# Performance work log

Measured on AMD Instinct MI355X. Metric: run time of the kernel, lower is better.

## Reference

```python
import jax, jax.numpy as jnp
import numpy as np

B, S, D, H = 2, 2048, 1024, 16
HD = D // H  # head_dim = 64


def setup_inputs() -> dict:
    key = jax.random.key(0)
    ks = jax.random.split(key, 6)
    sc = 1.0 / np.sqrt(D)
    x = jax.random.normal(ks[0], (B, S, D), dtype=jnp.float32)
    # causal boolean mask, broadcast over heads: [B, 1, S, S]
    causal = jnp.tril(jnp.ones((S, S), dtype=bool))
    attn_mask = jnp.broadcast_to(causal[None, None], (B, 1, S, S))
    return {
        "x": x,
        "attn_mask": attn_mask,
        "Wq": jax.random.normal(ks[1], (D, D), dtype=jnp.float32) * sc,
        "bq": jnp.zeros((D,), dtype=jnp.float32),
        "Wk": jax.random.normal(ks[2], (D, D), dtype=jnp.float32) * sc,
        "bk": jnp.zeros((D,), dtype=jnp.float32),
        "Wv": jax.random.normal(ks[3], (D, D), dtype=jnp.float32) * sc,
        "bv": jnp.zeros((D,), dtype=jnp.float32),
        "Wo": jax.random.normal(ks[4], (D, D), dtype=jnp.float32) * sc,
        "bo": jnp.zeros((D,), dtype=jnp.float32),
    }


def _split_heads(t):
    # [B, S, D] -> [B, H, S, HD]
    return t.reshape(B, S, H, HD).transpose(0, 2, 1, 3)


def reference(x, attn_mask, Wq, bq, Wk, bk, Wv, bv, Wo, bo):
    q = _split_heads(x @ Wq + bq)
    k = _split_heads(x @ Wk + bk)
    v = _split_heads(x @ Wv + bv)
    scale = 1.0 / jnp.sqrt(jnp.asarray(HD, dtype=x.dtype))
    # [B, H, S, S] scores
    scores = jnp.einsum("bhqd,bhkd->bhqk", q, k) * scale
    scores = jnp.where(attn_mask, scores, jnp.asarray(-jnp.inf, dtype=x.dtype))
    probs = jax.nn.softmax(scores, axis=-1)
    out = jnp.einsum("bhqk,bhkd->bhqd", probs, v)  # [B, H, S, HD]
    out = out.transpose(0, 2, 1, 3).reshape(B, S, D)
    return out @ Wo + bo
```

## Files before the change

### kernel.cpp

```cpp
#include <hip/hip_runtime.h>
#include <math.h>

#define BB 2
#define SS 2048
#define DDIM 1024
#define HH 16
#define HD 64
#define MM (BB * SS)

typedef short s16x8 __attribute__((ext_vector_type(8)));
typedef short s16x4 __attribute__((ext_vector_type(4)));
typedef float f32x4 __attribute__((ext_vector_type(4)));
typedef unsigned int u32x4 __attribute__((ext_vector_type(4)));

__device__ __forceinline__ unsigned short f2bf(float f) {
    unsigned int u = __builtin_bit_cast(unsigned int, f);
    u += 0x7fffu + ((u >> 16) & 1u);
    return (unsigned short)(u >> 16);
}
__device__ __forceinline__ float bf2f(unsigned short h) {
    return __builtin_bit_cast(float, (unsigned int)h << 16);
}

__global__ __launch_bounds__(256) void wsplit(
    const float* __restrict__ W0, const float* __restrict__ W1,
    const float* __restrict__ W2, const float* __restrict__ W3,
    short* __restrict__ WtH, short* __restrict__ WtL)
{
    __shared__ float T[64][65];
    const int z  = blockIdx.z;
    const float* W = (z == 0) ? W0 : (z == 1) ? W1 : (z == 2) ? W2 : W3;
    const int n0 = blockIdx.x * 64;
    const int k0 = blockIdx.y * 64;
    const int t  = threadIdx.x;

#pragma unroll
    for (int i = 0; i < 4; ++i) {
        const int kr = (t >> 4) + i * 16;
        const int c4 = (t & 15) * 4;
        const float4 v = *(const float4*)&W[(size_t)(k0 + kr) * DDIM + n0 + c4];
        T[kr][c4 + 0] = v.x; T[kr][c4 + 1] = v.y;
        T[kr][c4 + 2] = v.z; T[kr][c4 + 3] = v.w;
    }
    __syncthreads();

    const int n  = t >> 2;
    const int kb = (t & 3) * 16;
    s16x8 h0, h1, l0, l1;
#pragma unroll
    for (int j = 0; j < 8; ++j) {
        const float f0 = T[kb + j][n];
        const unsigned short hh0 = f2bf(f0);
        h0[j] = (short)hh0; l0[j] = (short)f2bf(f0 - bf2f(hh0));
        const float f1 = T[kb + 8 + j][n];
        const unsigned short hh1 = f2bf(f1);
        h1[j] = (short)hh1; l1[j] = (short)f2bf(f1 - bf2f(hh1));
    }
    const size_t ob = ((size_t)z * DDIM + n0 + n) * DDIM + k0 + kb;
    *(s16x8*)&WtH[ob]     = h0;
    *(s16x8*)&WtH[ob + 8] = h1;
    *(s16x8*)&WtL[ob]     = l0;
    *(s16x8*)&WtL[ob + 8] = l1;
}

template <int MODE>
__global__ __launch_bounds__(256) void proj_v2(
    const float* __restrict__ A, const short* __restrict__ BTh,
    const short* __restrict__ BTl, const float* __restrict__ bias,
    void* __restrict__ Cout)
{
    __shared__ short Bh[64 * 64];
    __shared__ short Bl[64 * 64];

    const int tid  = threadIdx.x;
    const int lane = tid & 63;
    const int wave = tid >> 6;
    const int g    = lane >> 4;
    const int qq   = lane & 15;
    const int wm   = (wave >> 1) * 32;
    const int wn   = (wave & 1) * 32;
    const int n0   = blockIdx.x * 64;
    const int m0   = blockIdx.y * 64;

    const int sr = tid >> 2;
    const int sc = (tid & 3) * 2;
    const int d0 = sr * 64 + ((sc ^ (sr & 7)) * 8);
    const int d1 = sr * 64 + (((sc + 1) ^ (sr & 7)) * 8);

    f32x4 acc[2][2];
#pragma unroll
    for (int i = 0; i < 2; ++i)
#pragma unroll
        for (int j = 0; j < 2; ++j) acc[i][j] = (f32x4){0.f, 0.f, 0.f, 0.f};

    for (int kt = 0; kt < 16; ++kt) {
        const int k0 = kt * 64;
        __syncthreads();
        {
            const size_t gb = (size_t)(n0 + sr) * DDIM + k0 + sc * 8;
            const s16x8 h0 = *(const s16x8*)&BTh[gb];
            const s16x8 h1 = *(const s16x8*)&BTh[gb + 8];
            const s16x8 l0 = *(const s16x8*)&BTl[gb];
            const s16x8 l1 = *(const s16x8*)&BTl[gb + 8];
            *(s16x8*)&Bh[d0] = h0;
            *(s16x8*)&Bh[d1] = h1;
            *(s16x8*)&Bl[d0] = l0;
            *(s16x8*)&Bl[d1] = l1;
        }
        __syncthreads();

#pragma unroll
        for (int ks = 0; ks < 2; ++ks) {
            s16x8 bhf[2], blf[2];
#pragma unroll
            for (int nf = 0; nf < 2; ++nf) {
                const int r  = wn + 16 * nf + qq;
                const int ch = (((ks * 4 + g) ^ (qq & 7)) * 8);
                bhf[nf] = *(const s16x8*)&Bh[r * 64 + ch];
                blf[nf] = *(const s16x8*)&Bl[r * 64 + ch];
            }
#pragma unroll
            for (int mf = 0; mf < 2; ++mf) {
                const float* ap = &A[(size_t)(m0 + wm + 16 * mf + qq) * DDIM + k0 + ks * 32 + g * 8];
                const float4 a0 = *(const float4*)ap;
                const float4 a1 = *(const float4*)(ap + 4);
                const float av[8] = {a0.x, a0.y, a0.z, a0.w, a1.x, a1.y, a1.z, a1.w};
                s16x8 ah, al;
#pragma unroll
                for (int i = 0; i < 8; ++i) {
                    const unsigned short hh = f2bf(av[i]);
                    ah[i] = (short)hh;
                    al[i] = (short)f2bf(av[i] - bf2f(hh));
                }
#pragma unroll
                for (int nf = 0; nf < 2; ++nf) {
                    acc[mf][nf] = __builtin_amdgcn_mfma_f32_16x16x32_bf16(ah, bhf[nf], acc[mf][nf], 0, 0, 0);
                    acc[mf][nf] = __builtin_amdgcn_mfma_f32_16x16x32_bf16(ah, blf[nf], acc[mf][nf], 0, 0, 0);
                    acc[mf][nf] = __builtin_amdgcn_mfma_f32_16x16x32_bf16(al, bhf[nf], acc[mf][nf], 0, 0, 0);
                }
            }
        }
    }

    float bv2[2];
#pragma unroll
    for (int nf = 0; nf < 2; ++nf) bv2[nf] = bias[n0 + wn + 16 * nf + qq];

#pragma unroll
    for (int mf = 0; mf < 2; ++mf) {
#pragma unroll
        for (int nf = 0; nf < 2; ++nf) {
            const int ncol = n0 + wn + 16 * nf + qq;
            if (MODE == 2) {
                const int mbase = m0 + wm + 16 * mf + 4 * g;
                const int b = mbase >> 11, s = mbase & 2047;
                const int h = ncol >> 6, d = ncol & 63;
                short p4[4];
#pragma unroll
                for (int r = 0; r < 4; ++r)
                    p4[r] = (short)f2bf(acc[mf][nf][r] + bv2[nf]);
                const s16x4 pv = {p4[0], p4[1], p4[2], p4[3]};
                *(s16x4*)&((short*)Cout)[(((size_t)(b * HH + h)) * HD + d) * SS + s] = pv;
            } else {
#pragma unroll
                for (int r = 0; r < 4; ++r) {
                    const int mrow = m0 + wm + 16 * mf + 4 * g + r;
                    const float val = acc[mf][nf][r] + bv2[nf];
                    if (MODE == 3) {
                        ((float*)Cout)[(size_t)mrow * DDIM + ncol] = val;
                    } else {
                        const int b = mrow >> 11, s = mrow & 2047;
                        const int h = ncol >> 6, d = ncol & 63;
                        if (MODE == 0) {
                            short* Q = (short*)Cout;
                            const size_t base = (((size_t)(b * HH + h)) * SS + s) * 128;
                            const unsigned short hh = f2bf(val);
                            Q[base + d]      = (short)hh;
                            Q[base + 64 + d] = (short)f2bf(val - bf2f(hh));
                        } else {
                            ((short*)Cout)[(((size_t)(b * HH + h)) * SS + s) * 64 + d] = (short)f2bf(val);
                        }
                    }
                }
            }
        }
    }
}

__global__ __launch_bounds__(256) void attn_mfma(
    const short* __restrict__ Qp, const short* __restrict__ Kp,
    const short* __restrict__ Vt, float* __restrict__ Ab)
{
    __shared__ short Kt[64 * 64];
    __shared__ short Vs[64 * 64];

    const int tid  = threadIdx.x;
    const int lane = tid & 63;
    const int wave = tid >> 6;
    const int g    = lane >> 4;
    const int qq   = lane & 15;
    const int qt   = 31 - blockIdx.x;
    const int h    = blockIdx.y;
    const int b    = blockIdx.z;
    const int q0   = qt * 64;
    const int qrow = q0 + wave * 16 + qq;

    const size_t headoff = (size_t)(b * HH + h) * SS;

    s16x8 qf[2][2];
#pragma unroll
    for (int half = 0; half < 2; ++half)
#pragma unroll
        for (int ks2 = 0; ks2 < 2; ++ks2)
            qf[half][ks2] = *(const s16x8*)&Qp[(headoff + qrow) * 128 + half * 64 + ks2 * 32 + g * 8];

    f32x4 oacc[4];
#pragma unroll
    for (int i = 0; i < 4; ++i) oacc[i] = (f32x4){0.f, 0.f, 0.f, 0.f};
    float mrun = -INFINITY, lrun = 0.f;

    for (int kt = 0; kt <= qt; ++kt) {
        const int kc0 = kt * 64;
        __syncthreads();
#pragma unroll
        for (int uu = 0; uu < 2; ++uu) {
            const int S = uu * 256 + tid;
            const int row = S >> 3, sl = S & 7;
            const int dsl = (sl ^ (row & 7)) * 8;
            const s16x8 kv = *(const s16x8*)&Kp[(headoff + kc0 + row) * 64 + sl * 8];
            *(s16x8*)&Kt[row * 64 + dsl] = kv;
            const s16x8 vv = *(const s16x8*)&Vt[((size_t)(b * HH + h) * HD + row) * SS + kc0 + sl * 8];
            *(s16x8*)&Vs[row * 64 + dsl] = vv;
        }
        __syncthreads();

        f32x4 sacc[4];
#pragma unroll
        for (int i = 0; i < 4; ++i) sacc[i] = (f32x4){0.f, 0.f, 0.f, 0.f};
#pragma unroll
        for (int kcf = 0; kcf < 4; ++kcf) {
            const int row = kcf * 16 + qq;
            s16x8 kf[2];
#pragma unroll
            for (int ks2 = 0; ks2 < 2; ++ks2)
                kf[ks2] = *(const s16x8*)&Kt[row * 64 + (((ks2 * 4 + g) ^ (row & 7)) * 8)];
#pragma unroll
            for (int half = 0; half < 2; ++half)
#pragma unroll
                for (int ks2 = 0; ks2 < 2; ++ks2)
                    sacc[kcf] = __builtin_amdgcn_mfma_f32_16x16x32_bf16(kf[ks2], qf[half][ks2], sacc[kcf], 0, 0, 0);
        }

        float sc[16];
        float pmax = -INFINITY;
#pragma unroll
        for (int kcf = 0; kcf < 4; ++kcf)
#pragma unroll
            for (int r = 0; r < 4; ++r) {
                float v = sacc[kcf][r] * 0.125f;
                const int kc = kc0 + kcf * 16 + g * 4 + r;
                if (kc > qrow) v = -INFINITY;
                sc[kcf * 4 + r] = v;
                pmax = fmaxf(pmax, v);
            }
        pmax = fmaxf(pmax, __shfl_xor(pmax, 16));
        pmax = fmaxf(pmax, __shfl_xor(pmax, 32));
        const float mnew  = fmaxf(mrun, pmax);
        const float alpha = __expf(mrun - mnew);
        float p[16], psum = 0.f;
#pragma unroll
        for (int i = 0; i < 16; ++i) { p[i] = __expf(sc[i] - mnew); psum += p[i]; }
        psum += __shfl_xor(psum, 16);
        psum += __shfl_xor(psum, 32);
        lrun = lrun * alpha + psum;
        mrun = mnew;
#pragma unroll
        for (int df = 0; df < 4; ++df) oacc[df] *= alpha;

        unsigned int pk[4][2];
#pragma unroll
        for (int kcf = 0; kcf < 4; ++kcf)
#pragma unroll
            for (int hh = 0; hh < 2; ++hh)
                pk[kcf][hh] = (unsigned int)f2bf(p[kcf * 4 + 2 * hh]) |
                              ((unsigned int)f2bf(p[kcf * 4 + 2 * hh + 1]) << 16);

        s16x8 pb[2];
#pragma unroll
        for (int ks = 0; ks < 2; ++ks) {
            unsigned int w_[4];
#pragma unroll
            for (int w = 0; w < 2 * 2; ++w) {
                const int gs  = (2 * g + (w >> 1)) & 3;
                const int src = qq | (gs << 4);
                const unsigned int va = (unsigned int)__shfl((int)pk[2 * ks][w & 1], src);
                const unsigned int vb = (unsigned int)__shfl((int)pk[2 * ks + 1][w & 1], src);
                w_[w] = (g & 2) ? vb : va;
            }
            const u32x4 t = {w_[0], w_[1], w_[2], w_[3]};
            pb[ks] = __builtin_bit_cast(s16x8, t);
        }

#pragma unroll
        for (int df = 0; df < 4; ++df) {
            const int row = df * 16 + qq;
#pragma unroll
            for (int ks = 0; ks < 2; ++ks) {
                const s16x8 vf = *(const s16x8*)&Vs[row * 64 + (((ks * 4 + g) ^ (row & 7)) * 8)];
                oacc[df] = __builtin_amdgcn_mfma_f32_16x16x32_bf16(vf, pb[ks], oacc[df], 0, 0, 0);
            }
        }
    }

    const float inv = 1.0f / lrun;
#pragma unroll
    for (int df = 0; df < 4; ++df) {
        f32x4 r = oacc[df];
        r *= inv;
        *(f32x4*)&Ab[((size_t)b * SS + qrow) * DDIM + h * HD + df * 16 + g * 4] = r;
    }
}

extern "C" void kernel_launch(void* const* d_in, const int* in_sizes, int n_in,
                              void* d_out, int out_size, void* d_ws, size_t ws_size,
                              hipStream_t stream)
{
    const float* x  = (const float*)d_in[0];
    const float* Wq = (const float*)d_in[2];
    const float* bq = (const float*)d_in[3];
    const float* Wk = (const float*)d_in[4];
    const float* bk = (const float*)d_in[5];
    const float* Wv = (const float*)d_in[6];
    const float* bv = (const float*)d_in[7];
    const float* Wo = (const float*)d_in[8];
    const float* bo = (const float*)d_in[9];
    float* out = (float*)d_out;

    char* w = (char*)d_ws;
    short* Kp  = (short*)w;
    short* Vt  = (short*)(w + (size_t) 8 * 1024 * 1024);
    float* Ab  = (float*)(w + (size_t)16 * 1024 * 1024);
    short* WtH = (short*)(w + (size_t)32 * 1024 * 1024);
    short* WtL = (short*)(w + (size_t)40 * 1024 * 1024);
    short* Qp  = (short*)d_out;

    const dim3 blk(256);
    const dim3 gg(DDIM / 64, MM / 64);

    wsplit<<<dim3(16, 16, 4), blk, 0, stream>>>(Wq, Wk, Wv, Wo, WtH, WtL);

    proj_v2<0><<<gg, blk, 0, stream>>>(x,  WtH + (size_t)0 * 1048576, WtL + (size_t)0 * 1048576, bq, (void*)Qp);
    proj_v2<1><<<gg, blk, 0, stream>>>(x,  WtH + (size_t)1 * 1048576, WtL + (size_t)1 * 1048576, bk, (void*)Kp);
    proj_v2<2><<<gg, blk, 0, stream>>>(x,  WtH + (size_t)2 * 1048576, WtL + (size_t)2 * 1048576, bv, (void*)Vt);

    attn_mfma<<<dim3(32, HH, BB), blk, 0, stream>>>(Qp, Kp, Vt, Ab);

    proj_v2<3><<<gg, blk, 0, stream>>>(Ab, WtH + (size_t)3 * 1048576, WtL + (size_t)3 * 1048576, bo, (void*)out);
}
```

Measured before the change: 498.4 us.

## Pre-split activations to bf16 hi/lo and drop LDS staging in projections

Adds an asplit kernel that converts the fp32 activations (x and the attention output) once into bf16 high/low halves in workspace, so the projection GEMMs no longer redo the split per tile. The projection kernel drops shared-memory staging of the weight tiles and its barriers, and each wave loads A and B fragments straight from global memory into MFMA operands. This removes repeated conversion ALU work and syncs, but adds extra launches and workspace traffic and loses LDS reuse of B across the waves in a block, which now rely on cache hits.

After: 670.7 us. 34.6% more time.

```diff
diff --git a/kernel.cpp b/kernel.cpp
--- a/kernel.cpp
+++ b/kernel.cpp
@@ -63,15 +63,30 @@
     *(s16x8*)&WtL[ob + 8] = l1;
 }
 
+__global__ __launch_bounds__(256) void asplit(
+    const float* __restrict__ X, short* __restrict__ XH, short* __restrict__ XL)
+{
+    const size_t i = ((size_t)blockIdx.x * 256 + threadIdx.x) * 8;
+    const float4 v0 = *(const float4*)&X[i];
+    const float4 v1 = *(const float4*)&X[i + 4];
+    const float f[8] = {v0.x, v0.y, v0.z, v0.w, v1.x, v1.y, v1.z, v1.w};
+    s16x8 h, l;
+#pragma unroll
+    for (int j = 0; j < 8; ++j) {
+        const unsigned short hh = f2bf(f[j]);
+        h[j] = (short)hh;
+        l[j] = (short)f2bf(f[j] - bf2f(hh));
+    }
+    *(s16x8*)&XH[i] = h;
+    *(s16x8*)&XL[i] = l;
+}
+
 template <int MODE>
-__global__ __launch_bounds__(256) void proj_v2(
-    const float* __restrict__ A, const short* __restrict__ BTh,
-    const short* __restrict__ BTl, const float* __restrict__ bias,
-    void* __restrict__ Cout)
-{
-    __shared__ short Bh[64 * 64];
-    __shared__ short Bl[64 * 64];
-
+__global__ __launch_bounds__(256) void proj_v3(
+    const short* __restrict__ AH, const short* __restrict__ AL,
+    const short* __restrict__ BTh, const short* __restrict__ BTl,
+    const float* __restrict__ bias, void* __restrict__ Cout)
+{
     const int tid  = threadIdx.x;
     const int lane = tid & 63;
     const int wave = tid >> 6;
@@ -82,10 +97,10 @@
     const int n0   = blockIdx.x * 64;
     const int m0   = blockIdx.y * 64;
 
-    const int sr = tid >> 2;
-    const int sc = (tid & 3) * 2;
-    const int d0 = sr * 64 + ((sc ^ (sr & 7)) * 8);
-    const int d1 = sr * 64 + (((sc + 1) ^ (sr & 7)) * 8);
+    const size_t ar0 = (size_t)(m0 + wm + qq) * DDIM;
+    const size_t ar1 = (size_t)(m0 + wm + 16 + qq) * DDIM;
+    const size_t br0 = (size_t)(n0 + wn + qq) * DDIM;
+    const size_t br1 = (size_t)(n0 + wn + 16 + qq) * DDIM;
 
     f32x4 acc[2][2];
 #pragma unroll
@@ -93,53 +108,30 @@
 #pragma unroll
         for (int j = 0; j < 2; ++j) acc[i][j] = (f32x4){0.f, 0.f, 0.f, 0.f};
 
-    for (int kt = 0; kt < 16; ++kt) {
-        const int k0 = kt * 64;
-        __syncthreads();
-        {
-            const size_t gb = (size_t)(n0 + sr) * DDIM + k0 + sc * 8;
-            const s16x8 h0 = *(const s16x8*)&BTh[gb];
-            const s16x8 h1 = *(const s16x8*)&BTh[gb + 8];
-            const s16x8 l0 = *(const s16x8*)&BTl[gb];
-            const s16x8 l1 = *(const s16x8*)&BTl[gb + 8];
-            *(s16x8*)&Bh[d0] = h0;
-            *(s16x8*)&Bh[d1] = h1;
-            *(s16x8*)&Bl[d0] = l0;
-            *(s16x8*)&Bl[d1] = l1;
-        }
-        __syncthreads();
-
-#pragma unroll
-        for (int ks = 0; ks < 2; ++ks) {
-            s16x8 bhf[2], blf[2];
-#pragma unroll
-            for (int nf = 0; nf < 2; ++nf) {
-                const int r  = wn + 16 * nf + qq;
-                const int ch = (((ks * 4 + g) ^ (qq & 7)) * 8);
-                bhf[nf] = *(const s16x8*)&Bh[r * 64 + ch];
-                blf[nf] = *(const s16x8*)&Bl[r * 64 + ch];
-            }
-#pragma unroll
-            for (int mf = 0; mf < 2; ++mf) {
-                const float* ap = &A[(size_t)(m0 + wm + 16 * mf + qq) * DDIM + k0 + ks * 32 + g * 8];
-                const float4 a0 = *(const float4*)ap;
-                const float4 a1 = *(const float4*)(ap + 4);
-                const float av[8] = {a0.x, a0.y, a0.z, a0.w, a1.x, a1.y, a1.z, a1.w};
-                s16x8 ah, al;
-#pragma unroll
-                for (int i = 0; i < 8; ++i) {
-                    const unsigned short hh = f2bf(av[i]);
-                    ah[i] = (short)hh;
-                    al[i] = (short)f2bf(av[i] - bf2f(hh));
-                }
-#pragma unroll
-                for (int nf = 0; nf < 2; ++nf) {
-                    acc[mf][nf] = __builtin_amdgcn_mfma_f32_16x16x32_bf16(ah, bhf[nf], acc[mf][nf], 0, 0, 0);
-                    acc[mf][nf] = __builtin_amdgcn_mfma_f32_16x16x32_bf16(ah, blf[nf], acc[mf][nf], 0, 0, 0);
-                    acc[mf][nf] = __builtin_amdgcn_mfma_f32_16x16x32_bf16(al, bhf[nf], acc[mf][nf], 0, 0, 0);
-                }
-            }
-        }
+#pragma unroll 2
+    for (int k0 = 0; k0 < DDIM; k0 += 32) {
+        const int kc = k0 + g * 8;
+        const s16x8 ah0 = *(const s16x8*)&AH[ar0 + kc];
+        const s16x8 al0 = *(const s16x8*)&AL[ar0 + kc];
+        const s16x8 ah1 = *(const s16x8*)&AH[ar1 + kc];
+        const s16x8 al1 = *(const s16x8*)&AL[ar1 + kc];
+        const s16x8 bh0 = *(const s16x8*)&BTh[br0 + kc];
+        const s16x8 bl0 = *(const s16x8*)&BTl[br0 + kc];
+        const s16x8 bh1 = *(const s16x8*)&BTh[br1 + kc];
+        const s16x8 bl1 = *(const s16x8*)&BTl[br1 + kc];
+
+        acc[0][0] = __builtin_amdgcn_mfma_f32_16x16x32_bf16(ah0, bh0, acc[0][0], 0, 0, 0);
+        acc[0][1] = __builtin_amdgcn_mfma_f32_16x16x32_bf16(ah0, bh1, acc[0][1], 0, 0, 0);
+        acc[1][0] = __builtin_amdgcn_mfma_f32_16x16x32_bf16(ah1, bh0, acc[1][0], 0, 0, 0);
+        acc[1][1] = __builtin_amdgcn_mfma_f32_16x16x32_bf16(ah1, bh1, acc[1][1], 0, 0, 0);
+        acc[0][0] = __builtin_amdgcn_mfma_f32_16x16x32_bf16(ah0, bl0, acc[0][0], 0, 0, 0);
+        acc[0][1] = __builtin_amdgcn_mfma_f32_16x16x32_bf16(ah0, bl1, acc[0][1], 0, 0, 0);
+        acc[1][0] = __builtin_amdgcn_mfma_f32_16x16x32_bf16(ah1, bl0, acc[1][0], 0, 0, 0);
+        acc[1][1] = __builtin_amdgcn_mfma_f32_16x16x32_bf16(ah1, bl1, acc[1][1], 0, 0, 0);
+        acc[0][0] = __builtin_amdgcn_mfma_f32_16x16x32_bf16(al0, bh0, acc[0][0], 0, 0, 0);
+        acc[0][1] = __builtin_amdgcn_mfma_f32_16x16x32_bf16(al0, bh1, acc[0][1], 0, 0, 0);
+        acc[1][0] = __builtin_amdgcn_mfma_f32_16x16x32_bf16(al1, bh0, acc[1][0], 0, 0, 0);
+        acc[1][1] = __builtin_amdgcn_mfma_f32_16x16x32_bf16(al1, bh1, acc[1][1], 0, 0, 0);
     }
 
     float bv2[2];
@@ -342,18 +334,23 @@
     float* Ab  = (float*)(w + (size_t)16 * 1024 * 1024);
     short* WtH = (short*)(w + (size_t)32 * 1024 * 1024);
     short* WtL = (short*)(w + (size_t)40 * 1024 * 1024);
+    short* AH  = (short*)(w + (size_t)48 * 1024 * 1024);
+    short* AL  = (short*)(w + (size_t)56 * 1024 * 1024);
     short* Qp  = (short*)d_out;
 
     const dim3 blk(256);
     const dim3 gg(DDIM / 64, MM / 64);
+    const int  asplit_blocks = MM * DDIM / (256 * 8);
 
     wsplit<<<dim3(16, 16, 4), blk, 0, stream>>>(Wq, Wk, Wv, Wo, WtH, WtL);
-
-    proj_v2<0><<<gg, blk, 0, stream>>>(x,  WtH + (size_t)0 * 1048576, WtL + (size_t)0 * 1048576, bq, (void*)Qp);
-    proj_v2<1><<<gg, blk, 0, stream>>>(x,  WtH + (size_t)1 * 1048576, WtL + (size_t)1 * 1048576, bk, (void*)Kp);
-    proj_v2<2><<<gg, blk, 0, stream>>>(x,  WtH + (size_t)2 * 1048576, WtL + (size_t)2 * 1048576, bv, (void*)Vt);
+    asplit<<<asplit_blocks, blk, 0, stream>>>(x, AH, AL);
+
+    proj_v3<0><<<gg, blk, 0, stream>>>(AH, AL, WtH + (size_t)0 * 1048576, WtL + (size_t)0 * 1048576, bq, (void*)Qp);
+    proj_v3<1><<<gg, blk, 0, stream>>>(AH, AL, WtH + (size_t)1 * 1048576, WtL + (size_t)1 * 1048576, bk, (void*)Kp);
+    proj_v3<2><<<gg, blk, 0, stream>>>(AH, AL, WtH + (size_t)2 * 1048576, WtL + (size_t)2 * 1048576, bv, (void*)Vt);
 
     attn_mfma<<<dim3(32, HH, BB), blk, 0, stream>>>(Qp, Kp, Vt, Ab);
 
-    proj_v2<3><<<gg, blk, 0, stream>>>(Ab, WtH + (size_t)3 * 1048576, WtL + (size_t)3 * 1048576, bo, (void*)out);
-}
+    asplit<<<asplit_blocks, blk, 0, stream>>>(Ab, AH, AL);
+    proj_v3<3><<<gg, blk, 0, stream>>>(AH, AL, WtH + (size_t)3 * 1048576, WtL + (size_t)3 * 1048576, bo, (void*)out);
+}
```
